# Kernel tuning notes

Measured on AMD Instinct MI355X. Metric: run time of the kernel, lower is better.

Reference implementation:

```python
import jax, jax.numpy as jnp
import numpy as np

N_NODES = 100000
N_EDGES = 3200000
F_IN = 512
HIDDEN = 16
N_CLASSES = 16


def setup_inputs() -> dict:
    key = jax.random.key(0)
    k1, k2, k3, k4 = jax.random.split(key, 4)
    x = jax.random.normal(k1, (N_NODES, F_IN), dtype=jnp.float32)
    edge_index = jax.random.randint(k2, (2, N_EDGES), 0, N_NODES, dtype=jnp.int32)
    # Glorot-style init for GCN weights
    W1 = jax.random.normal(k3, (F_IN, HIDDEN), dtype=jnp.float32) * np.float32(np.sqrt(2.0 / (F_IN + HIDDEN)))
    b1 = jnp.zeros((HIDDEN,), dtype=jnp.float32)
    W2 = jax.random.normal(k4, (HIDDEN, N_CLASSES), dtype=jnp.float32) * np.float32(np.sqrt(2.0 / (HIDDEN + N_CLASSES)))
    b2 = jnp.zeros((N_CLASSES,), dtype=jnp.float32)
    return {"x": x, "W1": W1, "b1": b1, "W2": W2, "b2": b2, "edge_index": edge_index}


def _gcn_conv(x, src, dst, W, b, n_nodes):
    """PyG GCNConv: h = x @ W, then symmetric-normalized aggregation with self-loops, + bias."""
    h = x @ W  # [N, out]
    # degrees include self-loops (edge weight 1.0 everywhere)
    ones = jnp.ones(src.shape[0], dtype=h.dtype)
    deg = jax.ops.segment_sum(ones, dst, num_segments=n_nodes) + 1.0  # +1 for self-loop
    dinv = jax.lax.rsqrt(deg)  # deg >= 1, no zero guard needed
    norm = dinv[src] * dinv[dst]  # [E]
    agg = jax.ops.segment_sum(h[src] * norm[:, None], dst, num_segments=n_nodes)
    # self-loop contribution: norm_ii = 1/deg_i
    agg = agg + h * (dinv * dinv)[:, None]
    return agg + b


def reference(x, W1, b1, W2, b2, edge_index):
    src, dst = edge_index[0], edge_index[1]
    n = x.shape[0]
    h = jax.nn.relu(_gcn_conv(x, src, dst, W1, b1, n))
    # dropout is identity in eval mode
    out = _gcn_conv(h, src, dst, W2, b2, n)
    return jax.nn.log_softmax(out, axis=1)
```

## Files before the change

kernel.cpp:

```cpp
#include <hip/hip_runtime.h>
#include <hip/hip_bf16.h>
#include <math.h>

constexpr int N_NODES = 100000;
constexpr int N_EDGES = 3200000;
constexpr int F_IN    = 512;
constexpr int HID     = 16;

constexpr int NPAD = 100352;

constexpr int B_BITS = 8;
constexpr int NPB    = 1 << B_BITS;
constexpr int NBKT   = (N_NODES + NPB - 1) / NPB;
constexpr int SBLK   = 400;
constexpr int CHUNK  = N_EDGES / SBLK;
constexpr int MAX_BKT_E = 12288;

__global__ __launch_bounds__(1024) void bin_count_kernel(const int* __restrict__ dst,
                                                         int* __restrict__ gcnt) {
    __shared__ int cnt[NBKT];
    const int tid = threadIdx.x;
    for (int t = tid; t < NBKT; t += 1024) cnt[t] = 0;
    __syncthreads();
    const int base = blockIdx.x * CHUNK;
    for (int i = tid; i < CHUNK; i += 1024)
        atomicAdd(&cnt[dst[base + i] >> B_BITS], 1);
    __syncthreads();
    for (int t = tid; t < NBKT; t += 1024)
        if (cnt[t]) atomicAdd(&gcnt[t], cnt[t]);
}

__global__ __launch_bounds__(512) void bucket_scan_kernel(const int* __restrict__ gcnt,
                                                          int* __restrict__ bbase,
                                                          int* __restrict__ gcur) {
    __shared__ int s[512];
    const int tid = threadIdx.x;
    s[tid] = (tid < NBKT) ? gcnt[tid] : 0;
    __syncthreads();
    for (int off = 1; off < 512; off <<= 1) {
        int v = (tid >= off) ? s[tid - off] : 0;
        __syncthreads();
        s[tid] += v;
        __syncthreads();
    }
    int excl = (tid == 0) ? 0 : s[tid - 1];
    if (tid <= NBKT) bbase[tid] = excl;
    if (tid <  NBKT) gcur[tid]  = excl;
}

__global__ __launch_bounds__(1024) void bin_scatter_kernel(const int* __restrict__ src,
                                                           const int* __restrict__ dst,
                                                           int* __restrict__ gcur,
                                                           unsigned int* __restrict__ binned) {
    __shared__ int cnt[NBKT];
    __shared__ int cur[NBKT];
    const int tid = threadIdx.x;
    for (int t = tid; t < NBKT; t += 1024) cnt[t] = 0;
    __syncthreads();
    const int base = blockIdx.x * CHUNK;
    for (int i = tid; i < CHUNK; i += 1024)
        atomicAdd(&cnt[dst[base + i] >> B_BITS], 1);
    __syncthreads();
    for (int t = tid; t < NBKT; t += 1024)
        cur[t] = cnt[t] ? atomicAdd(&gcur[t], cnt[t]) : 0;
    __syncthreads();
    for (int i = tid; i < CHUNK; i += 1024) {
        int d = dst[base + i];
        int b = d >> B_BITS;
        int pos = atomicAdd(&cur[b], 1);
        binned[pos] = ((unsigned)(d & (NPB - 1)) << 24) | (unsigned)src[base + i];
    }
}

__global__ __launch_bounds__(1024) void csr_bucket_kernel(const unsigned int* __restrict__ binned,
                                                          const int* __restrict__ bbase,
                                                          int* __restrict__ row,
                                                          int* __restrict__ csr,
                                                          float* __restrict__ dinv) {
    __shared__ unsigned int eb[MAX_BKT_E];
    __shared__ int deg[NPB];
    __shared__ int pre[NPB];
    __shared__ int cur[NPB];
    const int tid = threadIdx.x;
    const int b = blockIdx.x;
    const int e0 = bbase[b];
    int ne = bbase[b + 1] - e0;
    if (ne > MAX_BKT_E) ne = MAX_BKT_E;

    if (tid < NPB) deg[tid] = 0;
    for (int i = tid; i < ne; i += 1024) eb[i] = binned[e0 + i];
    __syncthreads();
    for (int i = tid; i < ne; i += 1024)
        atomicAdd(&deg[eb[i] >> 24], 1);
    __syncthreads();
    if (tid < NPB) pre[tid] = deg[tid];
    __syncthreads();
    for (int off = 1; off < NPB; off <<= 1) {
        int v = 0;
        if (tid < NPB && tid >= off) v = pre[tid - off];
        __syncthreads();
        if (tid < NPB) pre[tid] += v;
        __syncthreads();
    }
    if (tid < NPB) {
        int excl = (tid == 0) ? 0 : pre[tid - 1];
        int g = e0 + excl;
        cur[tid] = g;
        int node = b * NPB + tid;
        if (node < N_NODES) {
            row[node] = g;
            dinv[node] = rsqrtf((float)deg[tid] + 1.0f);
        }
    }
    if (b == 0 && tid == 0) row[N_NODES] = N_EDGES;
    __syncthreads();
    for (int i = tid; i < ne; i += 1024) {
        unsigned int v = eb[i];
        int pos = atomicAdd(&cur[v >> 24], 1);
        csr[pos] = (int)(v & 0xFFFFFFu);
    }
}

__global__ __launch_bounds__(256) void gemm1_kernel(const float* __restrict__ x,
                                                    const float* __restrict__ W1,
                                                    const float* __restrict__ b1,
                                                    const float* __restrict__ dinv,
                                                    float* __restrict__ hh,
                                                    float* __restrict__ agg1) {
    __shared__ float xs[16 * 512];
    __shared__ float w1s[3 * 2064 + 2048];
    const int tid = threadIdx.x;

    const float* gsrc = x + (size_t)blockIdx.x * 16 * F_IN;
    #pragma unroll
    for (int r = 0; r < 8; ++r) {
        int off = (r * 256 + tid) * 4;
        __builtin_amdgcn_global_load_lds(
            (const __attribute__((address_space(1))) void*)(gsrc + off),
            (__attribute__((address_space(3))) void*)(xs + off), 16, 0, 0);
    }
    for (int i = tid * 4; i < F_IN * HID; i += 256 * 4) {
        float4 v = *(const float4*)(W1 + i);
        int k = i >> 4, jw = i & 15;
        *(float4*)(w1s + (k >> 7) * 2064 + (k & 127) * 16 + jw) = v;
    }
    __syncthreads();

    const int wave = tid >> 6;
    const int lane = tid & 63;
    const int g = lane >> 4;
    const int j = lane & 15;
    const int node0 = blockIdx.x * 16 + wave * 4;

    const float* xr0 = xs + (wave * 4 + 0) * F_IN + g * 128;
    const float* xr1 = xs + (wave * 4 + 1) * F_IN + g * 128;
    const float* xr2 = xs + (wave * 4 + 2) * F_IN + g * 128;
    const float* xr3 = xs + (wave * 4 + 3) * F_IN + g * 128;
    const float* wg = w1s + g * 2064 + j;

    float acc0 = 0.f, acc1 = 0.f, acc2 = 0.f, acc3 = 0.f;
    const int rot = g << 1;
    #pragma unroll 4
    for (int t = 0; t < 32; ++t) {
        const int kk = ((t + rot) & 31) << 2;
        float4 a0 = *(const float4*)(xr0 + kk);
        float4 a1 = *(const float4*)(xr1 + kk);
        float4 a2 = *(const float4*)(xr2 + kk);
        float4 a3 = *(const float4*)(xr3 + kk);
        const float* wp = wg + kk * 16;
        float w0 = wp[0], w1v = wp[16], w2v = wp[32], w3v = wp[48];
        acc0 += a0.x * w0 + a0.y * w1v + a0.z * w2v + a0.w * w3v;
        acc1 += a1.x * w0 + a1.y * w1v + a1.z * w2v + a1.w * w3v;
        acc2 += a2.x * w0 + a2.y * w1v + a2.z * w2v + a2.w * w3v;
        acc3 += a3.x * w0 + a3.y * w1v + a3.z * w2v + a3.w * w3v;
    }
    acc0 += __shfl_xor(acc0, 16); acc0 += __shfl_xor(acc0, 32);
    acc1 += __shfl_xor(acc1, 16); acc1 += __shfl_xor(acc1, 32);
    acc2 += __shfl_xor(acc2, 16); acc2 += __shfl_xor(acc2, 32);
    acc3 += __shfl_xor(acc3, 16); acc3 += __shfl_xor(acc3, 32);

    if (g == 0) {
        float b1j = b1[j];
        float dv, hv;
        size_t o;
        dv = dinv[node0 + 0]; hv = acc0 * dv; o = (size_t)(node0 + 0) * 16 + j;
        hh[o] = hv; agg1[o] = hv * dv + b1j;
        dv = dinv[node0 + 1]; hv = acc1 * dv; o = (size_t)(node0 + 1) * 16 + j;
        hh[o] = hv; agg1[o] = hv * dv + b1j;
        dv = dinv[node0 + 2]; hv = acc2 * dv; o = (size_t)(node0 + 2) * 16 + j;
        hh[o] = hv; agg1[o] = hv * dv + b1j;
        dv = dinv[node0 + 3]; hv = acc3 * dv; o = (size_t)(node0 + 3) * 16 + j;
        hh[o] = hv; agg1[o] = hv * dv + b1j;
    }
}

__global__ __launch_bounds__(256) void pull_kernel(const float* __restrict__ hh,
                                                   const float* __restrict__ dinv,
                                                   const int* __restrict__ row,
                                                   const int* __restrict__ csr,
                                                   float* __restrict__ agg) {
    int t = blockIdx.x * 256 + threadIdx.x;
    int node = t >> 4;
    int j = t & 15;
    if (node >= N_NODES) return;
    int p = row[node], end = row[node + 1];
    float a0 = 0.f, a1 = 0.f, a2 = 0.f, a3 = 0.f;
    for (; p + 4 <= end; p += 4) {
        int s0 = csr[p], s1 = csr[p + 1], s2 = csr[p + 2], s3 = csr[p + 3];
        a0 += hh[(s0 << 4) + j];
        a1 += hh[(s1 << 4) + j];
        a2 += hh[(s2 << 4) + j];
        a3 += hh[(s3 << 4) + j];
    }
    for (; p < end; ++p) a0 += hh[(csr[p] << 4) + j];
    float acc = (a0 + a1) + (a2 + a3);
    agg[(node << 4) + j] += dinv[node] * acc;
}

__global__ __launch_bounds__(256) void layer2_kernel(const float* __restrict__ agg1,
                                                     const float* __restrict__ W2,
                                                     const float* __restrict__ b2,
                                                     const float* __restrict__ dinv,
                                                     float* __restrict__ hh2,
                                                     float* __restrict__ agg2) {
    __shared__ float w2s[256];
    __shared__ float b2s[16];
    const int tid = threadIdx.x;
    w2s[tid] = W2[tid];
    if (tid < 16) b2s[tid] = b2[tid];
    __syncthreads();
    int i = blockIdx.x * 256 + tid;
    if (i >= N_NODES) return;
    float v[16];
    const float4* ar = (const float4*)(agg1 + (size_t)i * 16);
    float4 r0 = ar[0], r1 = ar[1], r2 = ar[2], r3 = ar[3];
    v[0]=r0.x; v[1]=r0.y; v[2]=r0.z; v[3]=r0.w;
    v[4]=r1.x; v[5]=r1.y; v[6]=r1.z; v[7]=r1.w;
    v[8]=r2.x; v[9]=r2.y; v[10]=r2.z; v[11]=r2.w;
    v[12]=r3.x; v[13]=r3.y; v[14]=r3.z; v[15]=r3.w;
    #pragma unroll
    for (int k = 0; k < 16; ++k) v[k] = fmaxf(v[k], 0.f);
    float dv = dinv[i], dv2 = dv * dv;
    float o[16];
    #pragma unroll
    for (int jj = 0; jj < 16; ++jj) {
        float s = 0.f;
        #pragma unroll
        for (int k = 0; k < 16; ++k) s += v[k] * w2s[k * 16 + jj];
        o[jj] = s;
    }
    float4* ho = (float4*)(hh2 + (size_t)i * 16);
    float4* ao = (float4*)(agg2 + (size_t)i * 16);
    ho[0] = make_float4(o[0]*dv,  o[1]*dv,  o[2]*dv,  o[3]*dv);
    ho[1] = make_float4(o[4]*dv,  o[5]*dv,  o[6]*dv,  o[7]*dv);
    ho[2] = make_float4(o[8]*dv,  o[9]*dv,  o[10]*dv, o[11]*dv);
    ho[3] = make_float4(o[12]*dv, o[13]*dv, o[14]*dv, o[15]*dv);
    ao[0] = make_float4(o[0]*dv2+b2s[0],  o[1]*dv2+b2s[1],  o[2]*dv2+b2s[2],  o[3]*dv2+b2s[3]);
    ao[1] = make_float4(o[4]*dv2+b2s[4],  o[5]*dv2+b2s[5],  o[6]*dv2+b2s[6],  o[7]*dv2+b2s[7]);
    ao[2] = make_float4(o[8]*dv2+b2s[8],  o[9]*dv2+b2s[9],  o[10]*dv2+b2s[10],o[11]*dv2+b2s[11]);
    ao[3] = make_float4(o[12]*dv2+b2s[12],o[13]*dv2+b2s[13],o[14]*dv2+b2s[14],o[15]*dv2+b2s[15]);
}

__global__ __launch_bounds__(256) void lsm_kernel(const float* __restrict__ agg2,
                                                  float* __restrict__ out) {
    int i = blockIdx.x * 256 + threadIdx.x;
    if (i >= N_NODES) return;
    float v[16];
    const float4* ar = (const float4*)(agg2 + (size_t)i * 16);
    float4 r0 = ar[0], r1 = ar[1], r2 = ar[2], r3 = ar[3];
    v[0]=r0.x; v[1]=r0.y; v[2]=r0.z; v[3]=r0.w;
    v[4]=r1.x; v[5]=r1.y; v[6]=r1.z; v[7]=r1.w;
    v[8]=r2.x; v[9]=r2.y; v[10]=r2.z; v[11]=r2.w;
    v[12]=r3.x; v[13]=r3.y; v[14]=r3.z; v[15]=r3.w;
    float m = v[0];
    #pragma unroll
    for (int k = 1; k < 16; ++k) m = fmaxf(m, v[k]);
    float ssum = 0.f;
    #pragma unroll
    for (int k = 0; k < 16; ++k) ssum += expf(v[k] - m);
    float l = m + logf(ssum);
    float4* oo = (float4*)(out + (size_t)i * 16);
    oo[0] = make_float4(v[0]-l, v[1]-l, v[2]-l, v[3]-l);
    oo[1] = make_float4(v[4]-l, v[5]-l, v[6]-l, v[7]-l);
    oo[2] = make_float4(v[8]-l, v[9]-l, v[10]-l, v[11]-l);
    oo[3] = make_float4(v[12]-l, v[13]-l, v[14]-l, v[15]-l);
}

extern "C" void kernel_launch(void* const* d_in, const int* in_sizes, int n_in,
                              void* d_out, int out_size, void* d_ws, size_t ws_size,
                              hipStream_t stream) {
    const float* x    = (const float*)d_in[0];
    const float* W1   = (const float*)d_in[1];
    const float* b1   = (const float*)d_in[2];
    const float* W2   = (const float*)d_in[3];
    const float* b2   = (const float*)d_in[4];
    const int*   ei   = (const int*)d_in[5];
    const int*   src  = ei;
    const int*   dst  = ei + N_EDGES;
    float* out = (float*)d_out;

    int*   wsi  = (int*)d_ws;
    float* wsf  = (float*)d_ws;
    int*   gcnt  = wsi;
    int*   bbase = wsi + 512;
    int*   gcur  = wsi + 1024;
    float* dinv  = wsf + 2048;
    int*   row   = wsi + 2048 + NPAD;
    int*   csr   = wsi + 2048 + 2 * NPAD;
    unsigned int* binned = (unsigned int*)csr;
    float* hh    = wsf + 2048 + 2 * NPAD + N_EDGES;
    float* agg1  = hh   + (size_t)N_NODES * 16;
    float* hh2   = agg1 + (size_t)N_NODES * 16;
    float* agg2  = hh2  + (size_t)N_NODES * 16;

    const int NB = (N_NODES + 255) / 256;
    const int GB = N_NODES / 16;

    hipMemsetAsync(gcnt, 0, NBKT * sizeof(int), stream);
    bin_count_kernel <<<SBLK, 1024, 0, stream>>>(dst, gcnt);
    bucket_scan_kernel<<<1, 512, 0, stream>>>(gcnt, bbase, gcur);
    bin_scatter_kernel<<<SBLK, 1024, 0, stream>>>(src, dst, gcur, binned);
    csr_bucket_kernel<<<NBKT, 1024, 0, stream>>>(binned, bbase, row, csr, dinv);
    gemm1_kernel<<<GB, 256, 0, stream>>>(x, W1, b1, dinv, hh, agg1);
    pull_kernel<<<GB, 256, 0, stream>>>(hh, dinv, row, csr, agg1);
    layer2_kernel<<<NB, 256, 0, stream>>>(agg1, W2, b2, dinv, hh2, agg2);
    pull_kernel<<<GB, 256, 0, stream>>>(hh2, dinv, row, csr, agg2);
    lsm_kernel<<<NB, 256, 0, stream>>>(agg2, out);
}
```

Baseline: 495.8 us.

## Replace per-node CSR build with bucketed LDS-atomic aggregation

Drops the per-bucket CSR construction (local sort into row/csr arrays) and keeps only a degree count per bucket. Aggregation now runs one 1024-thread block per 256-node bucket over the binned edge list, accumulating into a shared-memory buffer with LDS float atomics before adding to the global output. This removes the CSR scatter pass and its extra writes, but it launches only about 391 blocks and adds atomic contention in shared memory. Floating-point summation order also becomes nondeterministic.

```diff
diff --git a/kernel.cpp b/kernel.cpp
--- a/kernel.cpp
+++ b/kernel.cpp
@@ -14,7 +14,6 @@
 constexpr int NBKT   = (N_NODES + NPB - 1) / NPB;
 constexpr int SBLK   = 400;
 constexpr int CHUNK  = N_EDGES / SBLK;
-constexpr int MAX_BKT_E = 12288;
 
 __global__ __launch_bounds__(1024) void bin_count_kernel(const int* __restrict__ dst,
                                                          int* __restrict__ gcnt) {
@@ -72,52 +71,21 @@
     }
 }
 
-__global__ __launch_bounds__(1024) void csr_bucket_kernel(const unsigned int* __restrict__ binned,
+__global__ __launch_bounds__(1024) void deg_bucket_kernel(const unsigned int* __restrict__ binned,
                                                           const int* __restrict__ bbase,
-                                                          int* __restrict__ row,
-                                                          int* __restrict__ csr,
                                                           float* __restrict__ dinv) {
-    __shared__ unsigned int eb[MAX_BKT_E];
     __shared__ int deg[NPB];
-    __shared__ int pre[NPB];
-    __shared__ int cur[NPB];
     const int tid = threadIdx.x;
     const int b = blockIdx.x;
-    const int e0 = bbase[b];
-    int ne = bbase[b + 1] - e0;
-    if (ne > MAX_BKT_E) ne = MAX_BKT_E;
-
     if (tid < NPB) deg[tid] = 0;
-    for (int i = tid; i < ne; i += 1024) eb[i] = binned[e0 + i];
-    __syncthreads();
-    for (int i = tid; i < ne; i += 1024)
-        atomicAdd(&deg[eb[i] >> 24], 1);
-    __syncthreads();
-    if (tid < NPB) pre[tid] = deg[tid];
-    __syncthreads();
-    for (int off = 1; off < NPB; off <<= 1) {
-        int v = 0;
-        if (tid < NPB && tid >= off) v = pre[tid - off];
-        __syncthreads();
-        if (tid < NPB) pre[tid] += v;
-        __syncthreads();
-    }
+    __syncthreads();
+    const int e0 = bbase[b], e1 = bbase[b + 1];
+    for (int e = e0 + tid; e < e1; e += 1024)
+        atomicAdd(&deg[binned[e] >> 24], 1);
+    __syncthreads();
     if (tid < NPB) {
-        int excl = (tid == 0) ? 0 : pre[tid - 1];
-        int g = e0 + excl;
-        cur[tid] = g;
-        int node = b * NPB + tid;
-        if (node < N_NODES) {
-            row[node] = g;
-            dinv[node] = rsqrtf((float)deg[tid] + 1.0f);
-        }
-    }
-    if (b == 0 && tid == 0) row[N_NODES] = N_EDGES;
-    __syncthreads();
-    for (int i = tid; i < ne; i += 1024) {
-        unsigned int v = eb[i];
-        int pos = atomicAdd(&cur[v >> 24], 1);
-        csr[pos] = (int)(v & 0xFFFFFFu);
+        int node = (b << B_BITS) + tid;
+        if (node < N_NODES) dinv[node] = rsqrtf((float)deg[tid] + 1.0f);
     }
 }
 
@@ -194,27 +162,35 @@
     }
 }
 
-__global__ __launch_bounds__(256) void pull_kernel(const float* __restrict__ hh,
-                                                   const float* __restrict__ dinv,
-                                                   const int* __restrict__ row,
-                                                   const int* __restrict__ csr,
-                                                   float* __restrict__ agg) {
-    int t = blockIdx.x * 256 + threadIdx.x;
-    int node = t >> 4;
-    int j = t & 15;
-    if (node >= N_NODES) return;
-    int p = row[node], end = row[node + 1];
-    float a0 = 0.f, a1 = 0.f, a2 = 0.f, a3 = 0.f;
-    for (; p + 4 <= end; p += 4) {
-        int s0 = csr[p], s1 = csr[p + 1], s2 = csr[p + 2], s3 = csr[p + 3];
-        a0 += hh[(s0 << 4) + j];
-        a1 += hh[(s1 << 4) + j];
-        a2 += hh[(s2 << 4) + j];
-        a3 += hh[(s3 << 4) + j];
-    }
-    for (; p < end; ++p) a0 += hh[(csr[p] << 4) + j];
-    float acc = (a0 + a1) + (a2 + a3);
-    agg[(node << 4) + j] += dinv[node] * acc;
+__global__ __launch_bounds__(1024) void pull_bucket_kernel(const unsigned int* __restrict__ binned,
+                                                           const int* __restrict__ bbase,
+                                                           const float* __restrict__ hh,
+                                                           const float* __restrict__ dinv,
+                                                           float* __restrict__ agg) {
+    __shared__ float acc[NPB * 16];
+    const int tid = threadIdx.x;
+    const int b = blockIdx.x;
+    const int j = tid & 15;
+    const int slot = tid >> 4;
+    for (int i = tid; i < NPB * 16; i += 1024) acc[i] = 0.f;
+    __syncthreads();
+    const int e0 = bbase[b], e1 = bbase[b + 1];
+    for (int e = e0 + slot; e < e1; e += 64) {
+        unsigned int v = binned[e];
+        int s  = (int)(v & 0xFFFFFFu);
+        int ld = (int)(v >> 24);
+        float val = hh[(s << 4) + j];
+        atomicAdd(&acc[(ld << 4) + j], val);
+    }
+    __syncthreads();
+    const int node0 = b << B_BITS;
+    for (int i = tid; i < NPB * 16; i += 1024) {
+        int node = node0 + (i >> 4);
+        if (node < N_NODES) {
+            size_t o = (size_t)node * 16 + (i & 15);
+            agg[o] += dinv[node] * acc[i];
+        }
+    }
 }
 
 __global__ __launch_bounds__(256) void layer2_kernel(const float* __restrict__ agg1,
@@ -305,10 +281,8 @@
     int*   bbase = wsi + 512;
     int*   gcur  = wsi + 1024;
     float* dinv  = wsf + 2048;
-    int*   row   = wsi + 2048 + NPAD;
-    int*   csr   = wsi + 2048 + 2 * NPAD;
-    unsigned int* binned = (unsigned int*)csr;
-    float* hh    = wsf + 2048 + 2 * NPAD + N_EDGES;
+    unsigned int* binned = (unsigned int*)(wsi + 2048 + NPAD);
+    float* hh    = wsf + 2048 + NPAD + N_EDGES;
     float* agg1  = hh   + (size_t)N_NODES * 16;
     float* hh2   = agg1 + (size_t)N_NODES * 16;
     float* agg2  = hh2  + (size_t)N_NODES * 16;
@@ -320,10 +294,10 @@
     bin_count_kernel <<<SBLK, 1024, 0, stream>>>(dst, gcnt);
     bucket_scan_kernel<<<1, 512, 0, stream>>>(gcnt, bbase, gcur);
     bin_scatter_kernel<<<SBLK, 1024, 0, stream>>>(src, dst, gcur, binned);
-    csr_bucket_kernel<<<NBKT, 1024, 0, stream>>>(binned, bbase, row, csr, dinv);
+    deg_bucket_kernel<<<NBKT, 1024, 0, stream>>>(binned, bbase, dinv);
     gemm1_kernel<<<GB, 256, 0, stream>>>(x, W1, b1, dinv, hh, agg1);
-    pull_kernel<<<GB, 256, 0, stream>>>(hh, dinv, row, csr, agg1);
+    pull_bucket_kernel<<<NBKT, 1024, 0, stream>>>(binned, bbase, hh, dinv, agg1);
     layer2_kernel<<<NB, 256, 0, stream>>>(agg1, W2, b2, dinv, hh2, agg2);
-    pull_kernel<<<GB, 256, 0, stream>>>(hh2, dinv, row, csr, agg2);
+    pull_bucket_kernel<<<NBKT, 1024, 0, stream>>>(binned, bbase, hh2, dinv, agg2);
     lsm_kernel<<<NB, 256, 0, stream>>>(agg2, out);
 }
```

Result: slower. 1.076 ms (+117.0%).
